# Kernel optimization log

Measured on AMD Instinct MI355X. Metric: run time of the kernel, lower is better.

Reference implementation:

```python
import jax, jax.numpy as jnp
import numpy as np

B, NT, NP, C, A = 8, 100, 300, 92, 64
EPS = 1e-7  # keras backend epsilon


def _lsa(cost):
    """Hungarian algorithm (Jonker-Volgenant style), cost [n, m] with n <= m.
    Equivalent to scipy.optimize.linear_sum_assignment."""
    n, m = cost.shape
    if n == 0:
        return np.zeros(0, np.int64), np.zeros(0, np.int64)
    u = np.zeros(n + 1)
    v = np.zeros(m + 1)
    p = np.zeros(m + 1, np.int64)
    way = np.zeros(m + 1, np.int64)
    for i in range(1, n + 1):
        p[0] = i
        j0 = 0
        minv = np.full(m + 1, np.inf)
        used = np.zeros(m + 1, bool)
        while True:
            used[j0] = True
            i0 = p[j0]
            cur = cost[i0 - 1] - u[i0] - v[1:]
            better = (~used[1:]) & (cur < minv[1:])
            minv[1:] = np.where(better, cur, minv[1:])
            way[1:] = np.where(better, j0, way[1:])
            cand = np.where(used[1:], np.inf, minv[1:])
            j1 = int(np.argmin(cand)) + 1
            delta = cand[j1 - 1]
            u[p[used]] += delta
            v[used] -= delta
            minv[~used] -= delta
            j0 = j1
            if p[j0] == 0:
                break
        while j0 != 0:
            j1 = way[j0]
            p[j0] = p[j1]
            j0 = j1
    cols = np.nonzero(p[1:])[0]
    rows = p[1:][cols] - 1
    return rows, cols


def _hungarian_mask(cost, num_objects):
    # mirrors MatchingAssignment.scipy_linear_assignment_mask
    masks = np.zeros(cost.shape, dtype=np.float32)
    for i in range(cost.shape[0]):
        n = int(num_objects[i])
        r, c = _lsa(cost[i, :n, :])
        masks[i][r, c] = 1.0
    return masks


def _focal(y, p):
    # tfa SigmoidFocalCrossEntropy: alpha=0.25, gamma=2.0, probabilities in
    p = jnp.clip(p, EPS, 1.0 - EPS)
    ce = -(y * jnp.log(p) + (1.0 - y) * jnp.log(1.0 - p))
    p_t = y * p + (1.0 - y) * (1.0 - p)
    alpha_f = y * 0.25 + (1.0 - y) * 0.75
    return jnp.sum(alpha_f * (1.0 - p_t) ** 2 * ce, -1)


def _iou_giou(b1, b2):
    # boxes are [ymin, xmin, ymax, xmax] (tfa convention)
    ay1, ax1, ay2, ax2 = b1[..., 0], b1[..., 1], b1[..., 2], b1[..., 3]
    by1, bx1, by2, bx2 = b2[..., 0], b2[..., 1], b2[..., 2], b2[..., 3]
    area_a = jnp.maximum(ay2 - ay1, 0.0) * jnp.maximum(ax2 - ax1, 0.0)
    area_b = jnp.maximum(by2 - by1, 0.0) * jnp.maximum(bx2 - bx1, 0.0)
    inter = (jnp.maximum(jnp.minimum(ay2, by2) - jnp.maximum(ay1, by1), 0.0)
             * jnp.maximum(jnp.minimum(ax2, bx2) - jnp.maximum(ax1, bx1), 0.0))
    union = area_a + area_b - inter
    iou = jnp.where(union > 0, inter / jnp.where(union > 0, union, 1.0), 0.0)
    enc = (jnp.maximum(jnp.maximum(ay2, by2) - jnp.minimum(ay1, by1), 0.0)
           * jnp.maximum(jnp.maximum(ax2, bx2) - jnp.minimum(ax1, bx1), 0.0))
    giou = iou - jnp.where(enc > 0, (enc - union) / jnp.where(enc > 0, enc, 1.0), 0.0)
    return iou, giou


def _cost_arrays(category, attribute, bbox, cat_preds, attribute_preds, box_preds):
    # CostArray: true -> [B,Nt,1,D], pred -> [B,1,Np,D], broadcast -> [B,Nt,Np]
    t_cat = category[:, :, None, :]
    p_cat = cat_preds[:, None, :, :]
    cat_match = jnp.sum((1.0 - p_cat) * t_cat, -1)
    cat_cost = -jnp.sum(jnp.log(p_cat + 1e-5) * t_cat, -1)
    attr_cost = _focal(attribute[:, :, None, :], attribute_preds[:, None, :, :])
    b_t = bbox[:, :, None, :]
    b_p = box_preds[:, None, :, :]
    iou, giou = _iou_giou(b_t, b_p)
    box_cost = 2.0 * (1.0 - giou) + 5.0 * jnp.mean(jnp.abs(b_t - b_p), -1)
    iou_arr = 1.0 - iou  # tfa GIoULoss(mode='iou') returns 1 - iou
    return cat_match, cat_cost, attr_cost, box_cost, iou_arr


def setup_inputs():
    key = jax.random.key(0)
    ks = jax.random.split(key, 9)
    category = jax.nn.one_hot(jax.random.randint(ks[0], (B, NT), 0, C), C, dtype=jnp.float32)
    attribute = (jax.random.uniform(ks[1], (B, NT, A)) < 0.3).astype(jnp.float32)
    yx = jax.random.uniform(ks[2], (B, NT, 2), maxval=0.8)
    hw = jax.random.uniform(ks[3], (B, NT, 2), minval=0.05, maxval=0.2)
    bbox = jnp.concatenate([yx, yx + hw], -1)
    num_objects = jax.random.randint(ks[4], (B,), 1, NT + 1).astype(jnp.int32)
    cat_preds = jax.nn.softmax(jax.random.normal(ks[5], (B, NP, C)), -1)
    attribute_preds = jax.nn.sigmoid(jax.random.normal(ks[6], (B, NP, A)))
    yxp = jax.random.uniform(ks[7], (B, NP, 2), maxval=0.8)
    hwp = jax.random.uniform(ks[8], (B, NP, 2), minval=0.05, maxval=0.2)
    box_preds = jnp.concatenate([yxp, yxp + hwp], -1)
    return dict(category=category, attribute=attribute, bbox=bbox,
                num_objects=num_objects, cat_preds=cat_preds,
                attribute_preds=attribute_preds, box_preds=box_preds)


def reference(category, attribute, bbox, num_objects, cat_preds, attribute_preds, box_preds):
    cat_match, cat_cost_arr, attr_cost_arr, box_cost_arr, iou_arr = _cost_arrays(
        category, attribute, bbox, cat_preds, attribute_preds, box_preds)

    # bipartite matching on CPU (mirrors tf.numpy_function + scipy)
    match_cost = np.asarray(cat_match + box_cost_arr, np.float64)
    mask = jnp.asarray(_hungarian_mask(match_cost, np.asarray(num_objects)))

    total_num_obj = jnp.sum(num_objects).astype(jnp.float32)
    total_num_preds = float(B * NP)

    category_cost = jnp.sum(mask * cat_cost_arr) / total_num_obj
    attribute_cost = jnp.sum(mask * attr_cost_arr) / total_num_obj
    box_cost = jnp.sum(mask * box_cost_arr) / total_num_obj

    # exist loss: keras CategoricalCrossentropy on single-channel probs
    assigned = jnp.max(mask, axis=1)[..., None]  # [B, Np, 1]
    yp = 1.0 - cat_preds[..., 0:1]
    pn = jnp.clip(yp / jnp.sum(yp, -1, keepdims=True), EPS, 1.0 - EPS)
    exist_loss = jnp.sum(-jnp.sum(assigned * jnp.log(pn), -1)) / total_num_preds

    total_loss = category_cost + attribute_cost + box_cost + exist_loss

    masked_iou = mask * iou_arr
    iou_metric = jnp.sum(masked_iou) / total_num_obj
    num_correct_50 = jnp.sum(masked_iou >= 0.5).astype(jnp.float32)
    map_50_95 = jnp.stack([jnp.sum(masked_iou >= r / 100.0).astype(jnp.float32)
                           for r in range(50, 100, 5)]).sum()
    num_predicted = jnp.sum(cat_preds[:, 1, :] < 0.5).astype(jnp.float32)
    mAP50 = num_correct_50 / num_predicted
    map_50_95 = map_50_95 / (num_predicted * 10.0)

    losses = jnp.stack([total_loss, category_cost, attribute_cost, box_cost, exist_loss])
    metrics = jnp.stack([iou_metric, mAP50, map_50_95])
    return losses, metrics
```

## Files before the change

kernel.cpp:

```cpp
#include <hip/hip_runtime.h>
#include <math.h>

#define Bb 8
#define NTt 100
#define NPp 300
#define Cc 92
#define Aa 64


__device__ __forceinline__ void iou_giou_f(const float* bt, const float* bp,
                                           float& iou, float& giou) {
  float ay1 = bt[0], ax1 = bt[1], ay2 = bt[2], ax2 = bt[3];
  float by1 = bp[0], bx1 = bp[1], by2 = bp[2], bx2 = bp[3];
  float area_a = fmaxf(ay2 - ay1, 0.0f) * fmaxf(ax2 - ax1, 0.0f);
  float area_b = fmaxf(by2 - by1, 0.0f) * fmaxf(bx2 - bx1, 0.0f);
  float inter = fmaxf(fminf(ay2, by2) - fmaxf(ay1, by1), 0.0f) *
                fmaxf(fminf(ax2, bx2) - fmaxf(ax1, bx1), 0.0f);
  float un = area_a + area_b - inter;
  iou = (un > 0.0f) ? (inter / un) : 0.0f;
  float enc = fmaxf(fmaxf(ay2, by2) - fminf(ay1, by1), 0.0f) *
              fmaxf(fmaxf(ax2, bx2) - fminf(ax1, bx1), 0.0f);
  giou = iou - ((enc > 0.0f) ? ((enc - un) / enc) : 0.0f);
}

__device__ __forceinline__ float box_cost_f(const float* bt, const float* bp,
                                            float& iou_out) {
  float iou, giou;
  iou_giou_f(bt, bp, iou, giou);
  iou_out = iou;
  float l1 = (fabsf(bt[0] - bp[0]) + fabsf(bt[1] - bp[1]) +
              fabsf(bt[2] - bp[2]) + fabsf(bt[3] - bp[3])) * 0.25f;
  return 2.0f * (1.0f - giou) + 5.0f * l1;
}


template <int CTRL>
__device__ __forceinline__ void dpp_fmin64(double& val) {
  union DU { double d; int i[2]; };
  DU a; a.d = val;
  int lo = __builtin_amdgcn_update_dpp(a.i[0], a.i[0], CTRL, 0xF, 0xF, false);
  int hi = __builtin_amdgcn_update_dpp(a.i[1], a.i[1], CTRL, 0xF, 0xF, false);
  DU o; o.i[0] = lo; o.i[1] = hi;
  val = fmin(val, o.d);
}

template <int CTRL>
__device__ __forceinline__ void dpp_step4(double& a, double& b, double& c, double& d) {
  dpp_fmin64<CTRL>(a); dpp_fmin64<CTRL>(b); dpp_fmin64<CTRL>(c); dpp_fmin64<CTRL>(d);
}

template <int CTRL>
__device__ __forceinline__ void dpp_umin32(unsigned int& val) {
  unsigned int o = (unsigned int)__builtin_amdgcn_update_dpp(
      (int)val, (int)val, CTRL, 0xF, 0xF, false);
  val = (o < val) ? o : val;
}

__device__ __forceinline__ unsigned int wave_umin32_bcast(unsigned int x) {
  dpp_umin32<0x111>(x);
  dpp_umin32<0x112>(x);
  dpp_umin32<0x114>(x);
  dpp_umin32<0x118>(x);
  dpp_umin32<0x142>(x);
  dpp_umin32<0x143>(x);
  return (unsigned int)__builtin_amdgcn_readlane((int)x, 63);
}

__device__ __forceinline__ double lane63_bcast(double x) {
  union DU { double d; int i[2]; };
  DU w; w.d = x;
  DU r;
  r.i[0] = __builtin_amdgcn_readlane(w.i[0], 63);
  r.i[1] = __builtin_amdgcn_readlane(w.i[1], 63);
  return r.d;
}

__device__ __forceinline__ double wave_fmin64_bcast(double m01) {
  double mv = m01;
  dpp_fmin64<0x111>(mv);
  dpp_fmin64<0x112>(mv);
  dpp_fmin64<0x114>(mv);
  dpp_fmin64<0x118>(mv);
  dpp_fmin64<0x142>(mv);
  dpp_fmin64<0x143>(mv);
  return lane63_bcast(mv);
}

__device__ __forceinline__ double read_u_row(double u_lo, double u_hi, int i0u) {
  int ridx = i0u - 1;
  int src = ridx & 63;
  union DU { double d; int i[2]; };
  DU a, bb, r;
  a.d = u_lo; bb.d = u_hi;
  int lo0 = __builtin_amdgcn_readlane(a.i[0], src);
  int hi0 = __builtin_amdgcn_readlane(a.i[1], src);
  int lo1 = __builtin_amdgcn_readlane(bb.i[0], src);
  int hi1 = __builtin_amdgcn_readlane(bb.i[1], src);
  bool hih = (ridx >> 6) != 0;
  r.i[0] = hih ? lo1 : lo0;
  r.i[1] = hih ? hi1 : hi0;
  return r.d;
}

__device__ __forceinline__ int sel5(int s, int a0, int a1, int a2, int a3, int a4) {
  int r = a4;
  r = (s == 3) ? a3 : r;
  r = (s == 2) ? a2 : r;
  r = (s == 1) ? a1 : r;
  r = (s == 0) ? a0 : r;
  return r;
}


__global__ void __launch_bounds__(64) cost_kernel(
    const float* __restrict__ category, const float* __restrict__ bbox,
    const float* __restrict__ box_preds, const float* __restrict__ cat_preds,
    float* __restrict__ cost, int* __restrict__ cls,
    float* __restrict__ rowminf, int* __restrict__ rowargj) {
  int bt = blockIdx.x;
  int b = bt / NTt;
  int lane = threadIdx.x;

  const float* crow = category + (size_t)bt * Cc;
  float c0 = (lane < Cc) ? crow[lane] : 0.0f;
  float c1 = (lane < Cc - 64) ? crow[lane + 64] : 0.0f;
  unsigned long long m0 = __ballot(c0 == 1.0f);
  unsigned long long m1 = __ballot(c1 == 1.0f);
  int cl = m0 ? __builtin_ctzll(m0) : (m1 ? 64 + __builtin_ctzll(m1) : 0);
  if (lane == 0) cls[bt] = cl;

  float tb[4];
  tb[0] = bbox[(size_t)bt * 4 + 0];
  tb[1] = bbox[(size_t)bt * 4 + 1];
  tb[2] = bbox[(size_t)bt * 4 + 2];
  tb[3] = bbox[(size_t)bt * 4 + 3];

  const float4* bp4 = (const float4*)(box_preds + (size_t)b * NPp * 4);
  const float* cp = cat_preds + (size_t)b * NPp * Cc + cl;
  float* crow_out = cost + (size_t)bt * NPp;

  float lmin = __builtin_inff();
  int   larg = 0x7FFFFFFF;

  #pragma unroll
  for (int k = 0; k < 5; ++k) {
    int p = lane + (k << 6);
    if (p < NPp) {
      float4 bpv = bp4[p];
      float pb[4] = {bpv.x, bpv.y, bpv.z, bpv.w};
      float iou;
      float bc = box_cost_f(tb, pb, iou);
      float pc = cp[(size_t)p * Cc];
      float cv = (1.0f - pc) + bc;
      crow_out[p] = cv;
      if (cv < lmin) { lmin = cv; larg = p; }
    }
  }

  union FU { float f; unsigned int u; };
  FU fu; fu.f = lmin;
  unsigned int minbits = wave_umin32_bcast(fu.u);
  unsigned int cand = (fu.u == minbits) ? (unsigned int)larg : 0xFFFFFFFFu;
  unsigned int argj = wave_umin32_bcast(cand);

  if (lane == 0) {
    FU mb; mb.u = minbits;
    rowminf[bt] = mb.f;
    rowargj[bt] = (int)argj;
  }
}


template <bool STAGE>
__global__ void __launch_bounds__(256, 1) jv_kernel(
    const int* __restrict__ num_objects, const float* __restrict__ cat_preds,
    const float* __restrict__ gcost, const float* __restrict__ rowminf,
    const int* __restrict__ rowargj, int* __restrict__ pj_g,
    double* __restrict__ partials) {
  extern __shared__ char smem[];
  const int b = blockIdx.x;
  const int tid = threadIdx.x;
  const int lane = tid & 63;

  float* lds_cost = (float*)smem;
  const int n = num_objects[b];
  const float* costg = gcost + (size_t)b * NTt * NPp;

  if (STAGE) {
    const float4* s4 = (const float4*)costg;
    float4* d4 = (float4*)lds_cost;
    int n4 = n * (NPp / 4);
    for (int t = tid; t < n4; t += 256) d4[t] = s4[t];
  }
  __syncthreads();

  if (tid >= 64) return;

  const float* costb = STAGE ? lds_cost : costg;

  const double INF = __builtin_inf();
  const bool active = lane < 60;
  const int laneOff = active ? 5 * lane : 0;

  double v0 = 0.0, v1 = 0.0, v2 = 0.0, v3 = 0.0, v4 = 0.0;
  double u_lo = 0.0, u_hi = 0.0;
  int wp0 = 0, wp1 = 0, wp2 = 0, wp3 = 0, wp4 = 0;
  int occm = 0;

  float mf0 = (lane < n) ? rowminf[b * NTt + lane] : 0.0f;
  int   aj0 = (lane < n) ? rowargj[b * NTt + lane] : 0;
  float mf1 = (lane + 64 < n) ? rowminf[b * NTt + lane + 64] : 0.0f;
  int   aj1 = (lane + 64 < n) ? rowargj[b * NTt + lane + 64] : 0;

  unsigned long long M0 = 0, M1 = 0, M2 = 0, M3 = 0, M4 = 0;
  int i = 1;
  while (i <= n) {
    int ridx = i - 1;
    int j1 = (ridx >> 6) ? __builtin_amdgcn_readlane(aj1, ridx & 63)
                         : __builtin_amdgcn_readlane(aj0, ridx & 63);
    int ow = j1 / 5, sk = j1 - 5 * (j1 / 5);
    unsigned long long Ms = (sk == 0) ? M0 : (sk == 1) ? M1 :
                            (sk == 2) ? M2 : (sk == 3) ? M3 : M4;
    if ((Ms >> ow) & 1) break;
    if      (sk == 0) M0 |= 1ull << ow;
    else if (sk == 1) M1 |= 1ull << ow;
    else if (sk == 2) M2 |= 1ull << ow;
    else if (sk == 3) M3 |= 1ull << ow;
    else              M4 |= 1ull << ow;
    if (lane == ow) {
      occm |= 1 << sk;
      if      (sk == 0) wp0 = (wp0 & ~127) | i;
      else if (sk == 1) wp1 = (wp1 & ~127) | i;
      else if (sk == 2) wp2 = (wp2 & ~127) | i;
      else if (sk == 3) wp3 = (wp3 & ~127) | i;
      else              wp4 = (wp4 & ~127) | i;
    }
    if ((ridx & 63) == lane) {
      if (ridx >> 6) u_hi += (double)mf1; else u_lo += (double)mf0;
    }
    ++i;
  }

  while (i <= n) {
    int cnt = n - i + 1; if (cnt > 4) cnt = 4;

    double m[4]; int p01a[4];
    #pragma unroll
    for (int r = 0; r < 4; ++r) {
      int row = i + r; if (row > n) row = n;
      const float* rowp = costb + (row - 1) * NPp + laneOff;
      float ca = rowp[0], cb2 = rowp[1], cc = rowp[2], cd = rowp[3], ce = rowp[4];
      double cv0 = active ? (double)ca - v0 : INF;
      double cv1 = active ? (double)cb2 - v1 : INF;
      double cv2 = active ? (double)cc - v2 : INF;
      double cv3 = active ? (double)cd - v3 : INF;
      double cv4 = active ? (double)ce - v4 : INF;
      double m01 = fmin(fmin(fmin(cv0, cv1), fmin(cv2, cv3)), cv4);
      int k0 = (cv3 == m01) ? 3 : 4;
      k0 = (cv2 == m01) ? 2 : k0;
      k0 = (cv1 == m01) ? 1 : k0;
      k0 = (cv0 == m01) ? 0 : k0;
      m[r] = m01;
      p01a[r] = laneOff + k0 + 1;
    }
    double r0 = m[0], r1 = m[1], r2 = m[2], r3 = m[3];
    dpp_step4<0x111>(r0, r1, r2, r3);
    dpp_step4<0x112>(r0, r1, r2, r3);
    dpp_step4<0x114>(r0, r1, r2, r3);
    dpp_step4<0x118>(r0, r1, r2, r3);
    dpp_step4<0x142>(r0, r1, r2, r3);
    dpp_step4<0x143>(r0, r1, r2, r3);
    double dly[4]; int jw[4];
    {
      double rr[4] = {r0, r1, r2, r3};
      #pragma unroll
      for (int r = 0; r < 4; ++r) {
        double delta = lane63_bcast(rr[r]);
        unsigned long long hit = __ballot(m[r] == delta);
        int winlane = __builtin_ctzll(hit);
        dly[r] = delta;
        jw[r] = __builtin_amdgcn_readlane(p01a[r], winlane);
      }
    }

    int consumed = 0, fbrow = 0;
    double fb_delta = 0.0; int fb_j1 = 0;
    #pragma unroll
    for (int r = 0; r < 4; ++r) {
      if (r < cnt && fbrow == 0) {
        int row = i + r;
        int j1 = jw[r];
        int jm = j1 - 1, ow = jm / 5, sk = jm - 5 * (jm / 5);
        unsigned long long mset = __ballot((occm >> sk) & 1);
        bool occ = (mset >> ow) & 1;
        consumed = r + 1;
        if (!occ) {
          if (lane == ow) {
            occm |= 1 << sk;
            if      (sk == 0) wp0 = (wp0 & ~127) | row;
            else if (sk == 1) wp1 = (wp1 & ~127) | row;
            else if (sk == 2) wp2 = (wp2 & ~127) | row;
            else if (sk == 3) wp3 = (wp3 & ~127) | row;
            else              wp4 = (wp4 & ~127) | row;
          }
          int ridx = row - 1;
          if ((ridx & 63) == lane) {
            if (ridx >> 6) u_hi += dly[r]; else u_lo += dly[r];
          }
        } else {
          fbrow = row; fb_delta = dly[r]; fb_j1 = j1;
        }
      }
    }

    if (fbrow) {
      const double delta1 = fb_delta;
      const float* rowp1 = costb + (fbrow - 1) * NPp + laneOff;
      float fa1 = rowp1[0], fb1 = rowp1[1], fc1 = rowp1[2],
            fd1 = rowp1[3], fe1 = rowp1[4];
      double mv0 = (double)fa1 - v0;
      double mv1 = (double)fb1 - v1;
      double mv2 = (double)fc1 - v2;
      double mv3 = (double)fd1 - v3;
      double mv4 = (double)fe1 - v4;
      wp0 &= 127; wp1 &= 127; wp2 &= 127; wp3 &= 127; wp4 &= 127;
      int usedmask = 0, uf = 0;
      {
        int ridx = fbrow - 1;
        if ((ridx & 63) == lane) {
          uf = 1 << (ridx >> 6);
          if (ridx >> 6) u_hi += delta1; else u_lo += delta1;
        }
      }
      mv0 -= delta1; mv1 -= delta1; mv2 -= delta1; mv3 -= delta1; mv4 -= delta1;

      int jm0 = fb_j1 - 1, wl0 = jm0 / 5, sk0 = jm0 - 5 * wl0;
      if (lane == wl0) {
        usedmask = 1 << sk0;
        if      (sk0 == 0) mv0 = -INF;
        else if (sk0 == 1) mv1 = -INF;
        else if (sk0 == 2) mv2 = -INF;
        else if (sk0 == 3) mv3 = -INF;
        else               mv4 = -INF;
      }
      int o0 = __builtin_amdgcn_readlane(wp0, wl0),
          o1 = __builtin_amdgcn_readlane(wp1, wl0),
          o2 = __builtin_amdgcn_readlane(wp2, wl0),
          o3 = __builtin_amdgcn_readlane(wp3, wl0),
          o4 = __builtin_amdgcn_readlane(wp4, wl0);
      int i0u = sel5(sk0, o0 & 127, o1 & 127, o2 & 127, o3 & 127, o4 & 127);
      int j0u = fb_j1;

      while (true) {
        { int ridx = i0u - 1; if ((ridx & 63) == lane) uf |= 1 << (ridx >> 6); }

        const float* rowp = costb + (i0u - 1) * NPp + laneOff;
        float fa = rowp[0], fb = rowp[1], fc = rowp[2], fd = rowp[3], fe = rowp[4];
        double ui0 = read_u_row(u_lo, u_hi, i0u);

        {
          double cur = (double)fa - ui0 - v0;
          wp0 = (cur < mv0) ? ((j0u << 7) | (wp0 & 127)) : wp0;
          mv0 = fmin(mv0, cur);
        }
        {
          double cur = (double)fb - ui0 - v1;
          wp1 = (cur < mv1) ? ((j0u << 7) | (wp1 & 127)) : wp1;
          mv1 = fmin(mv1, cur);
        }
        {
          double cur = (double)fc - ui0 - v2;
          wp2 = (cur < mv2) ? ((j0u << 7) | (wp2 & 127)) : wp2;
          mv2 = fmin(mv2, cur);
        }
        {
          double cur = (double)fd - ui0 - v3;
          wp3 = (cur < mv3) ? ((j0u << 7) | (wp3 & 127)) : wp3;
          mv3 = fmin(mv3, cur);
        }
        {
          double cur = (double)fe - ui0 - v4;
          wp4 = (cur < mv4) ? ((j0u << 7) | (wp4 & 127)) : wp4;
          mv4 = fmin(mv4, cur);
        }

        double dv0 = (!active || (usedmask & 1))  ? INF : mv0;
        double dv1 = (!active || (usedmask & 2))  ? INF : mv1;
        double dv2 = (!active || (usedmask & 4))  ? INF : mv2;
        double dv3 = (!active || (usedmask & 8))  ? INF : mv3;
        double dv4 = (!active || (usedmask & 16)) ? INF : mv4;

        double mm = fmin(fmin(fmin(dv0, dv1), fmin(dv2, dv3)), dv4);
        int kk = (dv3 == mm) ? 3 : 4;
        kk = (dv2 == mm) ? 2 : kk;
        kk = (dv1 == mm) ? 1 : kk;
        kk = (dv0 == mm) ? 0 : kk;
        int pl2 = sel5(kk, wp0 & 127, wp1 & 127, wp2 & 127, wp3 & 127, wp4 & 127);
        int pk2 = ((laneOff + kk + 1) << 7) | pl2;

        double delta2 = wave_fmin64_bcast(mm);
        unsigned long long hit2 = __ballot(mm == delta2);
        int winlane2 = __builtin_ctzll(hit2);
        int wpk2 = __builtin_amdgcn_readlane(pk2, winlane2);
        int j1b = wpk2 >> 7, i1b = wpk2 & 127;

        if (uf & 1) u_lo += delta2;
        if (uf & 2) u_hi += delta2;
        v0 -= (usedmask & 1)  ? delta2 : 0.0;
        v1 -= (usedmask & 2)  ? delta2 : 0.0;
        v2 -= (usedmask & 4)  ? delta2 : 0.0;
        v3 -= (usedmask & 8)  ? delta2 : 0.0;
        v4 -= (usedmask & 16) ? delta2 : 0.0;
        mv0 -= delta2; mv1 -= delta2; mv2 -= delta2; mv3 -= delta2; mv4 -= delta2;

        int jm = j1b - 1;
        int wl = jm / 5;
        int sk = jm - 5 * wl;
        if (lane == wl) {
          usedmask |= 1 << sk;
          if      (sk == 0) mv0 = -INF;
          else if (sk == 1) mv1 = -INF;
          else if (sk == 2) mv2 = -INF;
          else if (sk == 3) mv3 = -INF;
          else              mv4 = -INF;
        }

        j0u = j1b; i0u = i1b;
        if (i0u == 0) break;
      }

      {
        int jj = j0u;
        int idx = jj - 1;
        int owner = idx / 5;
        int slot = idx - 5 * owner;
        int f0 = __builtin_amdgcn_readlane(wp0, owner),
            f1 = __builtin_amdgcn_readlane(wp1, owner),
            f2 = __builtin_amdgcn_readlane(wp2, owner),
            f3 = __builtin_amdgcn_readlane(wp3, owner),
            f4 = __builtin_amdgcn_readlane(wp4, owner);
        int wpv = sel5(slot, f0, f1, f2, f3, f4);
        int wayv = wpv >> 7;

        while (true) {
          int jp = wayv;
          int newv;
          int wayn = 0;
          if (jp != 0) {
            int idx2 = jp - 1;
            int owner2 = idx2 / 5;
            int slot2 = idx2 - 5 * owner2;
            int g0 = __builtin_amdgcn_readlane(wp0, owner2),
                g1 = __builtin_amdgcn_readlane(wp1, owner2),
                g2 = __builtin_amdgcn_readlane(wp2, owner2),
                g3 = __builtin_amdgcn_readlane(wp3, owner2),
                g4 = __builtin_amdgcn_readlane(wp4, owner2);
            int wpn = sel5(slot2, g0, g1, g2, g3, g4);
            wayn = wpn >> 7;
            newv = wpn & 127;
          } else {
            newv = fbrow;
          }
          if (lane == owner) {
            if      (slot == 0) wp0 = (wp0 & ~127) | newv;
            else if (slot == 1) wp1 = (wp1 & ~127) | newv;
            else if (slot == 2) wp2 = (wp2 & ~127) | newv;
            else if (slot == 3) wp3 = (wp3 & ~127) | newv;
            else                wp4 = (wp4 & ~127) | newv;
          }
          if (jp == 0) break;
          jj = jp;
          idx = jj - 1;
          owner = idx / 5;
          slot = idx - 5 * owner;
          wayv = wayn;
        }
      }

      occm = ((wp0 & 127) ? 1 : 0) | ((wp1 & 127) ? 2 : 0) |
             ((wp2 & 127) ? 4 : 0) | ((wp3 & 127) ? 8 : 0) |
             ((wp4 & 127) ? 16 : 0);
    }

    i += consumed;
  }

  if (active) {
    int base = b * 304;
    pj_g[base + 5 * lane + 1] = wp0 & 127;
    pj_g[base + 5 * lane + 2] = wp1 & 127;
    pj_g[base + 5 * lane + 3] = wp2 & 127;
    pj_g[base + 5 * lane + 4] = wp3 & 127;
    pj_g[base + 5 * lane + 5] = wp4 & 127;
  }

  const float* cpb1 = cat_preds + ((size_t)b * NPp + 1) * Cc;
  float q0 = (lane < Cc) ? cpb1[lane] : 1.0f;
  float q1 = (lane + 64 < Cc) ? cpb1[lane + 64] : 1.0f;
  unsigned long long mm0 = __ballot(q0 < 0.5f);
  unsigned long long mm1 = __ballot(q1 < 0.5f);
  if (lane == 0) partials[b * 8 + 7] = (double)(__popcll(mm0) + __popcll(mm1));
}


__global__ void __launch_bounds__(64) loss_kernel(
    const float* __restrict__ attribute, const float* __restrict__ bbox,
    const float* __restrict__ cat_preds, const float* __restrict__ attribute_preds,
    const float* __restrict__ box_preds, const int* __restrict__ gcls,
    const int* __restrict__ pj_g, double* __restrict__ colpart) {
  int gb = blockIdx.x;
  int b = gb / NPp;
  int j = gb - b * NPp;
  int lane = threadIdx.x;
  double* outp = colpart + (size_t)gb * 8;

  int prow = pj_g[b * 304 + j + 1];
  if (prow == 0) {
    if (lane < 8) outp[lane] = 0.0;
    return;
  }

  int t = prow - 1;
  int bt = b * NTt + t;

  const float EPSF = 1e-7f;
  const float HIF  = (float)(1.0 - 1e-7);

  float y = attribute[(size_t)bt * Aa + lane];
  float p = fminf(fmaxf(attribute_preds[(size_t)gb * Aa + lane], EPSF), HIF);
  float ce = -(y * logf(p) + (1.0f - y) * logf(1.0f - p));
  float pt = y * p + (1.0f - y) * (1.0f - p);
  float alpha = y * 0.25f + (1.0f - y) * 0.75f;
  float om = 1.0f - pt;
  double sattr = (double)(alpha * (om * om) * ce);
  #pragma unroll
  for (int off = 32; off >= 1; off >>= 1) sattr += __shfl_xor(sattr, off);

  if (lane == 0) {
    int cl = gcls[bt];
    float pc = cat_preds[(size_t)gb * Cc + cl];
    double scat = (double)(-logf(pc + 1e-5f));

    const float* btp = bbox + (size_t)bt * 4;
    const float* bpp = box_preds + (size_t)gb * 4;
    float iou;
    float bc = box_cost_f(btp, bpp, iou);
    float ia = 1.0f - iou;

    double c50 = (ia >= 0.5f) ? 1.0 : 0.0;
    double call = 0.0;
    for (int rr = 50; rr < 100; rr += 5) {
      float thr = (float)((double)rr / 100.0);
      if (ia >= thr) call += 1.0;
    }

    float yp = 1.0f - cat_preds[(size_t)gb * Cc + 0];
    float pn = yp / yp;
    pn = fminf(fmaxf(pn, EPSF), HIF);
    double sex = (double)(-logf(pn));

    outp[0] = scat;
    outp[1] = sattr;
    outp[2] = (double)bc;
    outp[3] = (double)ia;
    outp[4] = sex;
    outp[5] = c50;
    outp[6] = call;
    outp[7] = 0.0;
  }
}


__global__ void __launch_bounds__(64) combine1_kernel(
    const double* __restrict__ colpart, double* __restrict__ partials) {
  int bid = blockIdx.x;
  int b = bid / 7;
  int q = bid - b * 7;
  int lane = threadIdx.x;

  double s = 0.0;
  #pragma unroll
  for (int k = 0; k < 5; ++k) {
    int j = lane + (k << 6);
    if (j < NPp) s += colpart[((size_t)(b * NPp + j)) * 8 + q];
  }
  #pragma unroll
  for (int off = 32; off >= 1; off >>= 1) s += __shfl_xor(s, off);
  if (lane == 0) partials[b * 8 + q] = s;
}


__global__ void final_kernel(const double* __restrict__ partials,
                             const int* __restrict__ num_objects,
                             float* __restrict__ out) {
  if (threadIdx.x != 0) return;
  double t[8];
  #pragma unroll
  for (int q = 0; q < 8; ++q) t[q] = 0.0;
  for (int b = 0; b < Bb; ++b)
    for (int q = 0; q < 8; ++q) t[q] += partials[b * 8 + q];

  int s = 0;
  for (int b = 0; b < Bb; ++b) s += num_objects[b];
  float tno = (float)s;

  float category_cost  = (float)t[0] / tno;
  float attribute_cost = (float)t[1] / tno;
  float box_cost       = (float)t[2] / tno;
  float exist_loss     = (float)t[4] / (float)(Bb * NPp);
  float total = category_cost + attribute_cost + box_cost + exist_loss;
  float iou_metric = (float)t[3] / tno;
  float npredf = (float)t[7];
  float mAP50 = (float)t[5] / npredf;
  float m5095 = (float)t[6] / (npredf * 10.0f);

  out[0] = total;
  out[1] = category_cost;
  out[2] = attribute_cost;
  out[3] = box_cost;
  out[4] = exist_loss;
  out[5] = iou_metric;
  out[6] = mAP50;
  out[7] = m5095;
}


extern "C" void kernel_launch(void* const* d_in, const int* in_sizes, int n_in,
                              void* d_out, int out_size, void* d_ws, size_t ws_size,
                              hipStream_t stream) {
  const float* category        = (const float*)d_in[0];
  const float* attribute       = (const float*)d_in[1];
  const float* bbox            = (const float*)d_in[2];
  const int*   num_objects     = (const int*)d_in[3];
  const float* cat_preds       = (const float*)d_in[4];
  const float* attribute_preds = (const float*)d_in[5];
  const float* box_preds       = (const float*)d_in[6];
  float* out = (float*)d_out;

  double* partials = (double*)d_ws;
  int*    gcls     = (int*)((char*)d_ws + 512);
  float*  gcost    = (float*)((char*)d_ws + 4096);
  int*    pj_g     = (int*)((char*)d_ws + 964096);
  double* colpart  = (double*)((char*)d_ws + 973824);
  float*  rowminf  = (float*)((char*)d_ws + 1127424);
  int*    rowargj  = (int*)((char*)d_ws + 1130624);

  cost_kernel<<<Bb * NTt, 64, 0, stream>>>(category, bbox, box_preds, cat_preds,
                                           gcost, gcls, rowminf, rowargj);

  const int STAGED_LDS = NTt * NPp * 4;
  hipError_t e = hipFuncSetAttribute(
      reinterpret_cast<const void*>(&jv_kernel<true>),
      hipFuncAttributeMaxDynamicSharedMemorySize, STAGED_LDS);
  if (e == hipSuccess) {
    jv_kernel<true><<<Bb, 256, STAGED_LDS, stream>>>(num_objects, cat_preds,
                                                     gcost, rowminf, rowargj,
                                                     pj_g, partials);
  } else {
    jv_kernel<false><<<Bb, 256, 0, stream>>>(num_objects, cat_preds,
                                             gcost, rowminf, rowargj,
                                             pj_g, partials);
  }

  loss_kernel<<<Bb * NPp, 64, 0, stream>>>(attribute, bbox, cat_preds,
                                           attribute_preds, box_preds, gcls,
                                           pj_g, colpart);
  combine1_kernel<<<Bb * 7, 64, 0, stream>>>(colpart, partials);
  final_kernel<<<1, 64, 0, stream>>>(partials, num_objects, out);
}
```

Measured before the change: 102.1 us.

## Track touched columns to reuse precomputed row minima in the Hungarian fast path

Measured after the change: 100.8 us. No clear change (-1.3%).

```diff
diff --git a/kernel.cpp b/kernel.cpp
--- a/kernel.cpp
+++ b/kernel.cpp
@@ -42,11 +42,6 @@
   int hi = __builtin_amdgcn_update_dpp(a.i[1], a.i[1], CTRL, 0xF, 0xF, false);
   DU o; o.i[0] = lo; o.i[1] = hi;
   val = fmin(val, o.d);
-}
-
-template <int CTRL>
-__device__ __forceinline__ void dpp_step4(double& a, double& b, double& c, double& d) {
-  dpp_fmin64<CTRL>(a); dpp_fmin64<CTRL>(b); dpp_fmin64<CTRL>(c); dpp_fmin64<CTRL>(d);
 }
 
 template <int CTRL>
@@ -111,6 +106,17 @@
   return r;
 }
 
+__device__ __forceinline__ unsigned long long selm5(int s,
+    unsigned long long a0, unsigned long long a1, unsigned long long a2,
+    unsigned long long a3, unsigned long long a4) {
+  unsigned long long r = a4;
+  r = (s == 3) ? a3 : r;
+  r = (s == 2) ? a2 : r;
+  r = (s == 1) ? a1 : r;
+  r = (s == 0) ? a0 : r;
+  return r;
+}
+
 
 __global__ void __launch_bounds__(64) cost_kernel(
     const float* __restrict__ category, const float* __restrict__ bbox,
@@ -206,49 +212,58 @@
   double u_lo = 0.0, u_hi = 0.0;
   int wp0 = 0, wp1 = 0, wp2 = 0, wp3 = 0, wp4 = 0;
   int occm = 0;
+  unsigned long long M0 = 0, M1 = 0, M2 = 0, M3 = 0, M4 = 0;
+  unsigned long long S0 = 0, S1 = 0, S2 = 0, S3 = 0, S4 = 0;
 
   float mf0 = (lane < n) ? rowminf[b * NTt + lane] : 0.0f;
   int   aj0 = (lane < n) ? rowargj[b * NTt + lane] : 0;
   float mf1 = (lane + 64 < n) ? rowminf[b * NTt + lane + 64] : 0.0f;
   int   aj1 = (lane + 64 < n) ? rowargj[b * NTt + lane + 64] : 0;
 
-  unsigned long long M0 = 0, M1 = 0, M2 = 0, M3 = 0, M4 = 0;
   int i = 1;
   while (i <= n) {
     int ridx = i - 1;
-    int j1 = (ridx >> 6) ? __builtin_amdgcn_readlane(aj1, ridx & 63)
-                         : __builtin_amdgcn_readlane(aj0, ridx & 63);
-    int ow = j1 / 5, sk = j1 - 5 * (j1 / 5);
-    unsigned long long Ms = (sk == 0) ? M0 : (sk == 1) ? M1 :
-                            (sk == 2) ? M2 : (sk == 3) ? M3 : M4;
-    if ((Ms >> ow) & 1) break;
-    if      (sk == 0) M0 |= 1ull << ow;
-    else if (sk == 1) M1 |= 1ull << ow;
-    else if (sk == 2) M2 |= 1ull << ow;
-    else if (sk == 3) M3 |= 1ull << ow;
-    else              M4 |= 1ull << ow;
-    if (lane == ow) {
-      occm |= 1 << sk;
-      if      (sk == 0) wp0 = (wp0 & ~127) | i;
-      else if (sk == 1) wp1 = (wp1 & ~127) | i;
-      else if (sk == 2) wp2 = (wp2 & ~127) | i;
-      else if (sk == 3) wp3 = (wp3 & ~127) | i;
-      else              wp4 = (wp4 & ~127) | i;
-    }
-    if ((ridx & 63) == lane) {
-      if (ridx >> 6) u_hi += (double)mf1; else u_lo += (double)mf0;
-    }
-    ++i;
-  }
-
-  while (i <= n) {
-    int cnt = n - i + 1; if (cnt > 4) cnt = 4;
-
-    double m[4]; int p01a[4];
-    #pragma unroll
-    for (int r = 0; r < 4; ++r) {
-      int row = i + r; if (row > n) row = n;
-      const float* rowp = costb + (row - 1) * NPp + laneOff;
+    int src = ridx & 63;
+    bool hi = (ridx >> 6) != 0;
+
+    bool needfb = false;
+    double fb_delta = 0.0;
+    int fb_j1 = 0;
+
+    int j1z = hi ? __builtin_amdgcn_readlane(aj1, src)
+                 : __builtin_amdgcn_readlane(aj0, src);
+    int ow = j1z / 5, sk = j1z - 5 * (j1z / 5);
+    unsigned long long Sms = selm5(sk, S0, S1, S2, S3, S4);
+
+    if (!((Sms >> ow) & 1)) {
+      unsigned long long Ms = selm5(sk, M0, M1, M2, M3, M4);
+      if (!((Ms >> ow) & 1)) {
+        if      (sk == 0) M0 |= 1ull << ow;
+        else if (sk == 1) M1 |= 1ull << ow;
+        else if (sk == 2) M2 |= 1ull << ow;
+        else if (sk == 3) M3 |= 1ull << ow;
+        else              M4 |= 1ull << ow;
+        if (lane == ow) {
+          occm |= 1 << sk;
+          if      (sk == 0) wp0 = (wp0 & ~127) | i;
+          else if (sk == 1) wp1 = (wp1 & ~127) | i;
+          else if (sk == 2) wp2 = (wp2 & ~127) | i;
+          else if (sk == 3) wp3 = (wp3 & ~127) | i;
+          else              wp4 = (wp4 & ~127) | i;
+        }
+        if (src == lane) {
+          if (hi) u_hi += (double)mf1; else u_lo += (double)mf0;
+        }
+        ++i;
+        continue;
+      }
+      int fbbits = hi ? __builtin_amdgcn_readlane(__float_as_int(mf1), src)
+                      : __builtin_amdgcn_readlane(__float_as_int(mf0), src);
+      fb_delta = (double)__int_as_float(fbbits);
+      fb_j1 = j1z + 1;
+      needfb = true;
+    } else {
+      const float* rowp = costb + ridx * NPp + laneOff;
       float ca = rowp[0], cb2 = rowp[1], cc = rowp[2], cd = rowp[3], ce = rowp[4];
       double cv0 = active ? (double)ca - v0 : INF;
       double cv1 = active ? (double)cb2 - v1 : INF;
@@ -260,60 +275,41 @@
       k0 = (cv2 == m01) ? 2 : k0;
       k0 = (cv1 == m01) ? 1 : k0;
       k0 = (cv0 == m01) ? 0 : k0;
-      m[r] = m01;
-      p01a[r] = laneOff + k0 + 1;
+      int p01 = laneOff + k0 + 1;
+      double delta = wave_fmin64_bcast(m01);
+      unsigned long long hit = __ballot(m01 == delta);
+      int winlane = __builtin_ctzll(hit);
+      int j1b = __builtin_amdgcn_readlane(p01, winlane);
+      int jm = j1b - 1, ow2 = jm / 5, sk2 = jm - 5 * (jm / 5);
+      unsigned long long Ms2 = selm5(sk2, M0, M1, M2, M3, M4);
+      if (!((Ms2 >> ow2) & 1)) {
+        if      (sk2 == 0) M0 |= 1ull << ow2;
+        else if (sk2 == 1) M1 |= 1ull << ow2;
+        else if (sk2 == 2) M2 |= 1ull << ow2;
+        else if (sk2 == 3) M3 |= 1ull << ow2;
+        else              M4 |= 1ull << ow2;
+        if (lane == ow2) {
+          occm |= 1 << sk2;
+          if      (sk2 == 0) wp0 = (wp0 & ~127) | i;
+          else if (sk2 == 1) wp1 = (wp1 & ~127) | i;
+          else if (sk2 == 2) wp2 = (wp2 & ~127) | i;
+          else if (sk2 == 3) wp3 = (wp3 & ~127) | i;
+          else               wp4 = (wp4 & ~127) | i;
+        }
+        if (src == lane) {
+          if (hi) u_hi += delta; else u_lo += delta;
+        }
+        ++i;
+        continue;
+      }
+      fb_delta = delta;
+      fb_j1 = j1b;
+      needfb = true;
     }
-    double r0 = m[0], r1 = m[1], r2 = m[2], r3 = m[3];
-    dpp_step4<0x111>(r0, r1, r2, r3);
-    dpp_step4<0x112>(r0, r1, r2, r3);
-    dpp_step4<0x114>(r0, r1, r2, r3);
-    dpp_step4<0x118>(r0, r1, r2, r3);
-    dpp_step4<0x142>(r0, r1, r2, r3);
-    dpp_step4<0x143>(r0, r1, r2, r3);
-    double dly[4]; int jw[4];
+
+    int usedmask = 0;
     {
-      double rr[4] = {r0, r1, r2, r3};
-      #pragma unroll
-      for (int r = 0; r < 4; ++r) {
-        double delta = lane63_bcast(rr[r]);
-        unsigned long long hit = __ballot(m[r] == delta);
-        int winlane = __builtin_ctzll(hit);
-        dly[r] = delta;
-        jw[r] = __builtin_amdgcn_readlane(p01a[r], winlane);
-      }
-    }
-
-    int consumed = 0, fbrow = 0;
-    double fb_delta = 0.0; int fb_j1 = 0;
-    #pragma unroll
-    for (int r = 0; r < 4; ++r) {
-      if (r < cnt && fbrow == 0) {
-        int row = i + r;
-        int j1 = jw[r];
-        int jm = j1 - 1, ow = jm / 5, sk = jm - 5 * (jm / 5);
-        unsigned long long mset = __ballot((occm >> sk) & 1);
-        bool occ = (mset >> ow) & 1;
-        consumed = r + 1;
-        if (!occ) {
-          if (lane == ow) {
-            occm |= 1 << sk;
-            if      (sk == 0) wp0 = (wp0 & ~127) | row;
-            else if (sk == 1) wp1 = (wp1 & ~127) | row;
-            else if (sk == 2) wp2 = (wp2 & ~127) | row;
-            else if (sk == 3) wp3 = (wp3 & ~127) | row;
-            else              wp4 = (wp4 & ~127) | row;
-          }
-          int ridx = row - 1;
-          if ((ridx & 63) == lane) {
-            if (ridx >> 6) u_hi += dly[r]; else u_lo += dly[r];
-          }
-        } else {
-          fbrow = row; fb_delta = dly[r]; fb_j1 = j1;
-        }
-      }
-    }
-
-    if (fbrow) {
+      const int fbrow = i;
       const double delta1 = fb_delta;
       const float* rowp1 = costb + (fbrow - 1) * NPp + laneOff;
       float fa1 = rowp1[0], fb1 = rowp1[1], fc1 = rowp1[2],
@@ -324,12 +320,12 @@
       double mv3 = (double)fd1 - v3;
       double mv4 = (double)fe1 - v4;
       wp0 &= 127; wp1 &= 127; wp2 &= 127; wp3 &= 127; wp4 &= 127;
-      int usedmask = 0, uf = 0;
+      int uf = 0;
       {
-        int ridx = fbrow - 1;
-        if ((ridx & 63) == lane) {
-          uf = 1 << (ridx >> 6);
-          if (ridx >> 6) u_hi += delta1; else u_lo += delta1;
+        int rr2 = fbrow - 1;
+        if ((rr2 & 63) == lane) {
+          uf = 1 << (rr2 >> 6);
+          if (rr2 >> 6) u_hi += delta1; else u_lo += delta1;
         }
       }
       mv0 -= delta1; mv1 -= delta1; mv2 -= delta1; mv3 -= delta1; mv4 -= delta1;
@@ -352,7 +348,7 @@
       int j0u = fb_j1;
 
       while (true) {
-        { int ridx = i0u - 1; if ((ridx & 63) == lane) uf |= 1 << (ridx >> 6); }
+        { int rr2 = i0u - 1; if ((rr2 & 63) == lane) uf |= 1 << (rr2 >> 6); }
 
         const float* rowp = costb + (i0u - 1) * NPp + laneOff;
         float fa = rowp[0], fb = rowp[1], fc = rowp[2], fd = rowp[3], fe = rowp[4];
@@ -415,14 +411,14 @@
 
         int jm = j1b - 1;
         int wl = jm / 5;
-        int sk = jm - 5 * wl;
+        int sk3 = jm - 5 * wl;
         if (lane == wl) {
-          usedmask |= 1 << sk;
-          if      (sk == 0) mv0 = -INF;
-          else if (sk == 1) mv1 = -INF;
-          else if (sk == 2) mv2 = -INF;
-          else if (sk == 3) mv3 = -INF;
-          else              mv4 = -INF;
+          usedmask |= 1 << sk3;
+          if      (sk3 == 0) mv0 = -INF;
+          else if (sk3 == 1) mv1 = -INF;
+          else if (sk3 == 2) mv2 = -INF;
+          else if (sk3 == 3) mv3 = -INF;
+          else               mv4 = -INF;
         }
 
         j0u = j1b; i0u = i1b;
@@ -476,13 +472,23 @@
           wayv = wayn;
         }
       }
-
-      occm = ((wp0 & 127) ? 1 : 0) | ((wp1 & 127) ? 2 : 0) |
-             ((wp2 & 127) ? 4 : 0) | ((wp3 & 127) ? 8 : 0) |
-             ((wp4 & 127) ? 16 : 0);
     }
 
-    i += consumed;
+    occm = ((wp0 & 127) ? 1 : 0) | ((wp1 & 127) ? 2 : 0) |
+           ((wp2 & 127) ? 4 : 0) | ((wp3 & 127) ? 8 : 0) |
+           ((wp4 & 127) ? 16 : 0);
+    M0 = __ballot(occm & 1);
+    M1 = __ballot(occm & 2);
+    M2 = __ballot(occm & 4);
+    M3 = __ballot(occm & 8);
+    M4 = __ballot(occm & 16);
+    S0 |= __ballot(usedmask & 1);
+    S1 |= __ballot(usedmask & 2);
+    S2 |= __ballot(usedmask & 4);
+    S3 |= __ballot(usedmask & 8);
+    S4 |= __ballot(usedmask & 16);
+
+    ++i;
   }
 
   if (active) {
```
